# Optimization experiments

Measured on AMD Instinct MI355X. Metric: run time of the kernel, lower is better.

## Reference

```python
import jax, jax.numpy as jnp
import numpy as np

B, S, H, E, TOPK = 4, 4096, 2048, 128, 8


def setup_inputs() -> dict:
    key = jax.random.key(0)
    k1, k2 = jax.random.split(key)
    hidden_states = jax.random.normal(k1, (B, S, H), dtype=jnp.float32)
    weight = jax.random.normal(k2, (E, H), dtype=jnp.float32) * 0.02
    return {"hidden_states": hidden_states, "weight": weight, "top_k": TOPK}


def reference(hidden_states, weight, top_k):
    x = hidden_states.reshape(-1, weight.shape[1])              # [T, H]
    router_logits = jnp.einsum('th,eh->te', x, weight)          # [T, E]
    router_probs = jax.nn.softmax(router_logits.astype(jnp.float32), axis=-1)
    router_top_value, router_indices = jax.lax.top_k(router_probs, top_k)  # [T, K]
    router_top_value = router_top_value / jnp.sum(router_top_value, axis=-1, keepdims=True)
    router_top_value = router_top_value.astype(router_logits.dtype)
    return (router_logits, router_top_value, router_indices)
```

## Files before the change

### kernel.cpp

```cpp
#include <hip/hip_runtime.h>
#include <hip/hip_bf16.h>
#include <hip/hip_fp16.h>

#define NTOK 16384
#define HDIM 2048
#define NEXP 128
#define KSEL 8
#define NCAND 16
#define DELTA_GAP 1e-4f
#define LO_SCALE 2048.0f
#define LO_INV (1.0f/2048.0f)

typedef _Float16 half8  __attribute__((ext_vector_type(8)));
typedef float    f32x4  __attribute__((ext_vector_type(4)));

__global__ __launch_bounds__(256) void w_convert(
    const float* __restrict__ w, _Float16* __restrict__ whp, _Float16* __restrict__ wlp)
{
    const int e = blockIdx.x;
    const int k = threadIdx.x * 8;
    const float* src = w + (size_t)e * HDIM + k;
    const f32x4 v0 = *reinterpret_cast<const f32x4*>(src);
    const f32x4 v1 = *reinterpret_cast<const f32x4*>(src + 4);
    float vv[8] = {v0[0], v0[1], v0[2], v0[3], v1[0], v1[1], v1[2], v1[3]};
    half8 h, lo;
#pragma unroll
    for (int j = 0; j < 8; ++j) {
        const _Float16 hj = (_Float16)vv[j];
        h[j]  = hj;
        lo[j] = (_Float16)((vv[j] - (float)hj) * LO_SCALE);
    }
    const int ks = k >> 5;
    const int eg = e >> 4;
    const int l  = (e & 15) | (((k >> 3) & 3) << 4);
    const size_t di = ((size_t)(ks * 8 + eg) * 64 + l) * 8;
    *reinterpret_cast<half8*>(whp + di) = h;
    *reinterpret_cast<half8*>(wlp + di) = lo;
}

__global__ __launch_bounds__(256, 2) void gemm3_nolds(
    const float* __restrict__ x,
    const _Float16* __restrict__ whp, const _Float16* __restrict__ wlp,
    float* __restrict__ logits, float* __restrict__ topv, float* __restrict__ topi,
    int* __restrict__ cand, int* __restrict__ flag)
{
    __shared__ f32x4 red[4][2][8][64];

    const int tid = threadIdx.x;
    const int l   = tid & 63;
    const int q   = tid >> 6;
    const int t0  = blockIdx.x * 32;

    const float* xrow0 = x + (size_t)(t0 + (l & 15)) * HDIM + q * 512 + 8 * (l >> 4);
    const float* xrow1 = xrow0 + (size_t)16 * HDIM;
    const _Float16* wqh = whp + (size_t)q * 16 * 8 * 512;
    const _Float16* wql = wlp + (size_t)q * 16 * 8 * 512;

    f32x4 acc[2][8], acc2[2][8];
#pragma unroll
    for (int ms = 0; ms < 2; ++ms)
#pragma unroll
        for (int eg = 0; eg < 8; ++eg) {
            acc[ms][eg]  = (f32x4){0.f, 0.f, 0.f, 0.f};
            acc2[ms][eg] = (f32x4){0.f, 0.f, 0.f, 0.f};
        }

    f32x4 acur[2][2];
    acur[0][0] = *reinterpret_cast<const f32x4*>(xrow0);
    acur[0][1] = *reinterpret_cast<const f32x4*>(xrow0 + 4);
    acur[1][0] = *reinterpret_cast<const f32x4*>(xrow1);
    acur[1][1] = *reinterpret_cast<const f32x4*>(xrow1 + 4);

#pragma unroll 1
    for (int s = 0; s < 16; ++s) {
        half8 bh[8], bl[8];
#pragma unroll
        for (int eg = 0; eg < 8; ++eg) {
            bh[eg] = *reinterpret_cast<const half8*>(wqh + ((size_t)s * 8 + eg) * 512 + l * 8);
            bl[eg] = *reinterpret_cast<const half8*>(wql + ((size_t)s * 8 + eg) * 512 + l * 8);
        }

        f32x4 anxt[2][2];
        if (s + 1 < 16) {
            anxt[0][0] = *reinterpret_cast<const f32x4*>(xrow0 + (s + 1) * 32);
            anxt[0][1] = *reinterpret_cast<const f32x4*>(xrow0 + (s + 1) * 32 + 4);
            anxt[1][0] = *reinterpret_cast<const f32x4*>(xrow1 + (s + 1) * 32);
            anxt[1][1] = *reinterpret_cast<const f32x4*>(xrow1 + (s + 1) * 32 + 4);
        }

        half8 ah[2], al[2];
#pragma unroll
        for (int ms = 0; ms < 2; ++ms)
#pragma unroll
            for (int j = 0; j < 4; ++j) {
                const _Float16 h0 = (_Float16)acur[ms][0][j];
                const _Float16 h1 = (_Float16)acur[ms][1][j];
                ah[ms][j]     = h0;
                ah[ms][4 + j] = h1;
                al[ms][j]     = (_Float16)((acur[ms][0][j] - (float)h0) * LO_SCALE);
                al[ms][4 + j] = (_Float16)((acur[ms][1][j] - (float)h1) * LO_SCALE);
            }

#pragma unroll
        for (int eg = 0; eg < 8; ++eg)
#pragma unroll
            for (int ms = 0; ms < 2; ++ms) {
                acc[ms][eg]  = __builtin_amdgcn_mfma_f32_16x16x32_f16(ah[ms], bh[eg], acc[ms][eg],  0, 0, 0);
                acc2[ms][eg] = __builtin_amdgcn_mfma_f32_16x16x32_f16(ah[ms], bl[eg], acc2[ms][eg], 0, 0, 0);
                acc2[ms][eg] = __builtin_amdgcn_mfma_f32_16x16x32_f16(al[ms], bh[eg], acc2[ms][eg], 0, 0, 0);
            }

        if (s + 1 < 16) {
#pragma unroll
            for (int ms = 0; ms < 2; ++ms)
#pragma unroll
                for (int h = 0; h < 2; ++h)
                    acur[ms][h] = anxt[ms][h];
        }
    }

#pragma unroll
    for (int ms = 0; ms < 2; ++ms)
#pragma unroll
        for (int eg = 0; eg < 8; ++eg)
            red[q][ms][eg][l] = acc[ms][eg] + acc2[ms][eg] * LO_INV;
    __syncthreads();

    const int ms_w = q >> 1;
    f32x4 v[8];
#pragma unroll
    for (int eg = 0; eg < 8; ++eg) {
        f32x4 s0 = red[0][ms_w][eg][l];
        s0 += red[1][ms_w][eg][l];
        s0 += red[2][ms_w][eg][l];
        s0 += red[3][ms_w][eg][l];
        v[eg] = s0;
    }

    const int grp  = l >> 4;
    const int ln16 = l & 15;
    const int r0   = 2 * (q & 1);
    const float NEG = -__builtin_inff();

#pragma unroll
    for (int rr = 0; rr < 4; ++rr) {
        if (rr != r0 && rr != r0 + 1) continue;
        const int t = t0 + ms_w * 16 + 4 * grp + rr;
        float vr[8];
#pragma unroll
        for (int f = 0; f < 8; ++f) {
            vr[f] = v[f][rr];
            logits[(size_t)t * NEXP + 16 * f + ln16] = vr[f];
        }

        unsigned selm = 0u;
        int   mycand = 0;
        float mycv   = 0.0f;
#pragma unroll
        for (int k = 0; k < NCAND; ++k) {
            float lv = NEG; int le = 0;
#pragma unroll
            for (int f = 0; f < 8; ++f) {
                const float c = ((selm >> f) & 1u) ? NEG : vr[f];
                if (c > lv) { lv = c; le = 16 * f + ln16; }
            }
            float cv = lv; int ce = le;
#pragma unroll
            for (int off = 8; off > 0; off >>= 1) {
                const float ov = __shfl_xor(cv, off, 16);
                const int   oe = __shfl_xor(ce, off, 16);
                if (ov > cv || (ov == cv && oe < ce)) { cv = ov; ce = oe; }
            }
            if (ln16 == k) { mycand = ce; mycv = cv; }
            if ((ce & 15) == ln16) selm |= 1u << (ce >> 4);
        }

        const float nv = __shfl(mycv, ln16 + 1, 16);
        int fl = (ln16 <= 8 && (mycv - nv) < DELTA_GAP) ? 1 : 0;
#pragma unroll
        for (int off = 8; off > 0; off >>= 1)
            fl |= __shfl_xor(fl, off, 16);

        const float m = __shfl(mycv, 0, 16);
        const float p = (ln16 < KSEL) ? expf(mycv - m) : 0.0f;
        float ps = p;
#pragma unroll
        for (int off = 8; off > 0; off >>= 1)
            ps += __shfl_xor(ps, off, 16);

        cand[(size_t)t * NCAND + ln16] = mycand;
        if (ln16 < KSEL) {
            topv[(size_t)t * KSEL + ln16] = p / ps;
            topi[(size_t)t * KSEL + ln16] = (float)mycand;
        }
        if (ln16 == 0) flag[t] = fl;
    }
}

__global__ __launch_bounds__(256) void refine_flagged(
    const float* __restrict__ x, const float* __restrict__ w,
    const int* __restrict__ cand, const int* __restrict__ flag,
    float* __restrict__ topv, float* __restrict__ topi)
{
    const int l = threadIdx.x & 63;
    const int t = (int)((blockIdx.x * 256u + threadIdx.x) >> 6);
    if (!flag[t]) return;

    const int myid = cand[(size_t)t * NCAND + (l & 15)];
    const float* xrow = x + (size_t)t * HDIM;

    double xd[32];
#pragma unroll
    for (int i = 0; i < 8; ++i) {
        const f32x4 xv = *reinterpret_cast<const f32x4*>(xrow + i * 256 + l * 4);
#pragma unroll
        for (int j = 0; j < 4; ++j) xd[i * 4 + j] = (double)xv[j];
    }

    double part[NCAND];
    int    cid[NCAND];
#pragma unroll
    for (int c = 0; c < NCAND; ++c) {
        const int eid = __shfl(myid, c);
        cid[c] = eid;
        const float* wrow = w + (size_t)eid * HDIM;
        double s0 = 0.0, s1 = 0.0, s2 = 0.0, s3 = 0.0;
#pragma unroll
        for (int i = 0; i < 8; ++i) {
            const f32x4 wv4 = *reinterpret_cast<const f32x4*>(wrow + i * 256 + l * 4);
            s0 = fma(xd[i * 4 + 0], (double)wv4[0], s0);
            s1 = fma(xd[i * 4 + 1], (double)wv4[1], s1);
            s2 = fma(xd[i * 4 + 2], (double)wv4[2], s2);
            s3 = fma(xd[i * 4 + 3], (double)wv4[3], s3);
        }
        part[c] = (s0 + s1) + (s2 + s3);
    }

#pragma unroll
    for (int off = 32; off > 0; off >>= 1)
#pragma unroll
        for (int c = 0; c < NCAND; ++c)
            part[c] += __shfl_xor(part[c], off);

    unsigned selm = 0u;
    double m = 0.0, kv = 0.0;
    int ki = 0;
    float psum = 0.0f;
#pragma unroll
    for (int k = 0; k < KSEL; ++k) {
        double bv = -__builtin_inf(); int bi = 0x7fffffff; int bc = 0;
#pragma unroll
        for (int c = 0; c < NCAND; ++c) {
            if (!((selm >> c) & 1u)) {
                if (part[c] > bv || (part[c] == bv && cid[c] < bi)) {
                    bv = part[c]; bi = cid[c]; bc = c;
                }
            }
        }
        if (k == 0) m = bv;
        psum += expf((float)(bv - m));
        if (l == k) { kv = bv; ki = bi; }
        selm |= 1u << bc;
    }

    if (l < KSEL) {
        topv[(size_t)t * KSEL + l] = expf((float)(kv - m)) / psum;
        topi[(size_t)t * KSEL + l] = (float)ki;
    }
}

#define BM 64
#define BK 32
#define BSTRIDE (BK + 4)
__global__ __launch_bounds__(256) void router_fused(
    const float* __restrict__ x, const float* __restrict__ w,
    float* __restrict__ logits, float* __restrict__ topv, float* __restrict__ topi)
{
    __shared__ float Bs[NEXP][BSTRIDE];
    const int tid = threadIdx.x;
    const int tn = tid & 15, tm = tid >> 4;
    const int row0 = blockIdx.x * BM;
    const int kc = tid & 7, cr = tid >> 3;

    double acc[4][8];
#pragma unroll
    for (int i = 0; i < 4; ++i)
#pragma unroll
        for (int j = 0; j < 8; ++j) acc[i][j] = 0.0;

    const float* xp[4];
#pragma unroll
    for (int i = 0; i < 4; ++i) xp[i] = x + (size_t)(row0 + tm + 16 * i) * HDIM;

    float4 rb[4];
#pragma unroll
    for (int p = 0; p < 4; ++p)
        rb[p] = *reinterpret_cast<const float4*>(&w[(size_t)(cr + 32 * p) * HDIM + kc * 4]);

    for (int k0 = 0; k0 < HDIM; k0 += BK) {
        __syncthreads();
#pragma unroll
        for (int p = 0; p < 4; ++p)
            *reinterpret_cast<float4*>(&Bs[cr + 32 * p][kc * 4]) = rb[p];
        __syncthreads();
        if (k0 + BK < HDIM) {
#pragma unroll
            for (int p = 0; p < 4; ++p)
                rb[p] = *reinterpret_cast<const float4*>(
                    &w[(size_t)(cr + 32 * p) * HDIM + (k0 + BK) + kc * 4]);
        }
#pragma unroll 4
        for (int k4 = 0; k4 < BK; k4 += 4) {
            float4 a4[4], b4[8];
#pragma unroll
            for (int i = 0; i < 4; ++i)
                a4[i] = *reinterpret_cast<const float4*>(&xp[i][k0 + k4]);
#pragma unroll
            for (int j = 0; j < 8; ++j)
                b4[j] = *reinterpret_cast<const float4*>(&Bs[tn + 16 * j][k4]);
#pragma unroll
            for (int kk = 0; kk < 4; ++kk) {
                double bd[8];
#pragma unroll
                for (int j = 0; j < 8; ++j) bd[j] = (double)((const float*)&b4[j])[kk];
#pragma unroll
                for (int i = 0; i < 4; ++i) {
                    const double ad = (double)((const float*)&a4[i])[kk];
#pragma unroll
                    for (int j = 0; j < 8; ++j) acc[i][j] = fma(ad, bd[j], acc[i][j]);
                }
            }
        }
    }
#pragma unroll
    for (int i = 0; i < 4; ++i) {
        float* orow = logits + (size_t)(row0 + tm + 16 * i) * NEXP;
#pragma unroll
        for (int j = 0; j < 8; ++j) orow[tn + 16 * j] = (float)acc[i][j];
    }
    for (int i = 0; i < 4; ++i) {
        const int t = row0 + tm + 16 * i;
        unsigned sel = 0u;
        double m = 0.0, kv = 0.0;
        int ki = 0;
        const double NEGD = -__builtin_inf();
#pragma unroll
        for (int k = 0; k < KSEL; ++k) {
            double lv = NEGD; int le = 0;
#pragma unroll
            for (int j = 0; j < 8; ++j) {
                const double v = (sel >> j) & 1u ? NEGD : acc[i][j];
                if (v > lv) { lv = v; le = tn + 16 * j; }
            }
            double cv = lv; int ce = le;
#pragma unroll
            for (int off = 8; off > 0; off >>= 1) {
                const double ov = __shfl_xor(cv, off, 16);
                const int    oe = __shfl_xor(ce, off, 16);
                if (ov > cv || (ov == cv && oe < ce)) { cv = ov; ce = oe; }
            }
            if (k == 0) m = cv;
            if (tn == k) { kv = cv; ki = ce; }
            if ((ce & 15) == tn) sel |= 1u << (ce >> 4);
        }
        float z = 0.0f;
#pragma unroll
        for (int j = 0; j < 8; ++j) z += expf((float)(acc[i][j] - m));
#pragma unroll
        for (int off = 8; off > 0; off >>= 1) z += __shfl_xor(z, off, 16);
        const float p = (tn < KSEL) ? expf((float)(kv - m)) / z : 0.0f;
        float ps = p;
#pragma unroll
        for (int off = 8; off > 0; off >>= 1) ps += __shfl_xor(ps, off, 16);
        if (tn < KSEL) {
            topv[(size_t)t * KSEL + tn] = p / ps;
            topi[(size_t)t * KSEL + tn] = (float)ki;
        }
    }
}

extern "C" void kernel_launch(void* const* d_in, const int* in_sizes, int n_in,
                              void* d_out, int out_size, void* d_ws, size_t ws_size,
                              hipStream_t stream) {
    const float* x = (const float*)d_in[0];
    const float* w = (const float*)d_in[1];

    float* out    = (float*)d_out;
    float* logits = out;
    float* topv   = out + (size_t)NTOK * NEXP;
    float* topi   = topv + (size_t)NTOK * KSEL;

    const size_t plane = (size_t)NEXP * HDIM;
    const size_t need  = plane * 2 * sizeof(_Float16)
                       + (size_t)NTOK * NCAND * sizeof(int)
                       + (size_t)NTOK * sizeof(int);
    if (ws_size >= need) {
        _Float16* whp = (_Float16*)d_ws;
        _Float16* wlp = whp + plane;
        int* cand = (int*)(wlp + plane);
        int* flag = cand + (size_t)NTOK * NCAND;
        w_convert<<<NEXP, 256, 0, stream>>>(w, whp, wlp);
        gemm3_nolds<<<NTOK / 32, 256, 0, stream>>>(x, whp, wlp, logits, topv, topi, cand, flag);
        refine_flagged<<<NTOK / 4, 256, 0, stream>>>(x, w, cand, flag, topv, topi);
    } else {
        router_fused<<<NTOK / BM, 256, 0, stream>>>(x, w, logits, topv, topi);
    }
}
```

Measured before the change: 81.57 us.

## Split GEMM waves over expert halves and K halves to cut registers

Each wave previously covered all 128 experts over a quarter of K. It now covers 64 experts over half of K, which halves the accumulator registers and allows the launch bound to rise from 2 to 3 blocks per SM. The shared-memory reduction shrinks from a four-way sum to a two-way sum. The software prefetch of the next x slice is removed, and refine_flagged now keeps x as float and converts to double at each use, which further lowers register pressure. The risk is that each wave reads twice as many x values per MFMA and loses the load/compute overlap the prefetch provided.

```diff
diff --git a/kernel.cpp b/kernel.cpp
--- a/kernel.cpp
+++ b/kernel.cpp
@@ -38,109 +38,94 @@
     *reinterpret_cast<half8*>(wlp + di) = lo;
 }
 
-__global__ __launch_bounds__(256, 2) void gemm3_nolds(
+__global__ __launch_bounds__(256, 3) void gemm3_split(
     const float* __restrict__ x,
     const _Float16* __restrict__ whp, const _Float16* __restrict__ wlp,
     float* __restrict__ logits, float* __restrict__ topv, float* __restrict__ topi,
     int* __restrict__ cand, int* __restrict__ flag)
 {
-    __shared__ f32x4 red[4][2][8][64];
+    __shared__ f32x4 red[2][2][2][4][64];
 
     const int tid = threadIdx.x;
     const int l   = tid & 63;
-    const int q   = tid >> 6;
+    const int W   = tid >> 6;
+    const int eh  = W & 1;
+    const int kh  = W >> 1;
     const int t0  = blockIdx.x * 32;
 
-    const float* xrow0 = x + (size_t)(t0 + (l & 15)) * HDIM + q * 512 + 8 * (l >> 4);
+    const float* xrow0 = x + (size_t)(t0 + (l & 15)) * HDIM + kh * 1024 + 8 * (l >> 4);
     const float* xrow1 = xrow0 + (size_t)16 * HDIM;
-    const _Float16* wqh = whp + (size_t)q * 16 * 8 * 512;
-    const _Float16* wql = wlp + (size_t)q * 16 * 8 * 512;
-
-    f32x4 acc[2][8], acc2[2][8];
+
+    f32x4 acc[2][4], acc2[2][4];
 #pragma unroll
     for (int ms = 0; ms < 2; ++ms)
 #pragma unroll
-        for (int eg = 0; eg < 8; ++eg) {
-            acc[ms][eg]  = (f32x4){0.f, 0.f, 0.f, 0.f};
-            acc2[ms][eg] = (f32x4){0.f, 0.f, 0.f, 0.f};
-        }
-
-    f32x4 acur[2][2];
-    acur[0][0] = *reinterpret_cast<const f32x4*>(xrow0);
-    acur[0][1] = *reinterpret_cast<const f32x4*>(xrow0 + 4);
-    acur[1][0] = *reinterpret_cast<const f32x4*>(xrow1);
-    acur[1][1] = *reinterpret_cast<const f32x4*>(xrow1 + 4);
+        for (int g = 0; g < 4; ++g) {
+            acc[ms][g]  = (f32x4){0.f, 0.f, 0.f, 0.f};
+            acc2[ms][g] = (f32x4){0.f, 0.f, 0.f, 0.f};
+        }
 
 #pragma unroll 1
-    for (int s = 0; s < 16; ++s) {
-        half8 bh[8], bl[8];
-#pragma unroll
-        for (int eg = 0; eg < 8; ++eg) {
-            bh[eg] = *reinterpret_cast<const half8*>(wqh + ((size_t)s * 8 + eg) * 512 + l * 8);
-            bl[eg] = *reinterpret_cast<const half8*>(wql + ((size_t)s * 8 + eg) * 512 + l * 8);
-        }
-
-        f32x4 anxt[2][2];
-        if (s + 1 < 16) {
-            anxt[0][0] = *reinterpret_cast<const f32x4*>(xrow0 + (s + 1) * 32);
-            anxt[0][1] = *reinterpret_cast<const f32x4*>(xrow0 + (s + 1) * 32 + 4);
-            anxt[1][0] = *reinterpret_cast<const f32x4*>(xrow1 + (s + 1) * 32);
-            anxt[1][1] = *reinterpret_cast<const f32x4*>(xrow1 + (s + 1) * 32 + 4);
-        }
+    for (int s = 0; s < 32; ++s) {
+        const int ks = kh * 32 + s;
+
+        half8 bh[4], bl[4];
+#pragma unroll
+        for (int g = 0; g < 4; ++g) {
+            const size_t off = (size_t)(ks * 8 + 4 * eh + g) * 512 + l * 8;
+            bh[g] = *reinterpret_cast<const half8*>(whp + off);
+            bl[g] = *reinterpret_cast<const half8*>(wlp + off);
+        }
+
+        const f32x4 a00 = *reinterpret_cast<const f32x4*>(xrow0 + s * 32);
+        const f32x4 a01 = *reinterpret_cast<const f32x4*>(xrow0 + s * 32 + 4);
+        const f32x4 a10 = *reinterpret_cast<const f32x4*>(xrow1 + s * 32);
+        const f32x4 a11 = *reinterpret_cast<const f32x4*>(xrow1 + s * 32 + 4);
 
         half8 ah[2], al[2];
 #pragma unroll
-        for (int ms = 0; ms < 2; ++ms)
-#pragma unroll
-            for (int j = 0; j < 4; ++j) {
-                const _Float16 h0 = (_Float16)acur[ms][0][j];
-                const _Float16 h1 = (_Float16)acur[ms][1][j];
-                ah[ms][j]     = h0;
-                ah[ms][4 + j] = h1;
-                al[ms][j]     = (_Float16)((acur[ms][0][j] - (float)h0) * LO_SCALE);
-                al[ms][4 + j] = (_Float16)((acur[ms][1][j] - (float)h1) * LO_SCALE);
-            }
-
-#pragma unroll
-        for (int eg = 0; eg < 8; ++eg)
+        for (int j = 0; j < 4; ++j) {
+            const _Float16 h00 = (_Float16)a00[j];
+            const _Float16 h01 = (_Float16)a01[j];
+            const _Float16 h10 = (_Float16)a10[j];
+            const _Float16 h11 = (_Float16)a11[j];
+            ah[0][j]     = h00;
+            ah[0][4 + j] = h01;
+            ah[1][j]     = h10;
+            ah[1][4 + j] = h11;
+            al[0][j]     = (_Float16)((a00[j] - (float)h00) * LO_SCALE);
+            al[0][4 + j] = (_Float16)((a01[j] - (float)h01) * LO_SCALE);
+            al[1][j]     = (_Float16)((a10[j] - (float)h10) * LO_SCALE);
+            al[1][4 + j] = (_Float16)((a11[j] - (float)h11) * LO_SCALE);
+        }
+
+#pragma unroll
+        for (int g = 0; g < 4; ++g)
 #pragma unroll
             for (int ms = 0; ms < 2; ++ms) {
-                acc[ms][eg]  = __builtin_amdgcn_mfma_f32_16x16x32_f16(ah[ms], bh[eg], acc[ms][eg],  0, 0, 0);
-                acc2[ms][eg] = __builtin_amdgcn_mfma_f32_16x16x32_f16(ah[ms], bl[eg], acc2[ms][eg], 0, 0, 0);
-                acc2[ms][eg] = __builtin_amdgcn_mfma_f32_16x16x32_f16(al[ms], bh[eg], acc2[ms][eg], 0, 0, 0);
-            }
-
-        if (s + 1 < 16) {
-#pragma unroll
-            for (int ms = 0; ms < 2; ++ms)
-#pragma unroll
-                for (int h = 0; h < 2; ++h)
-                    acur[ms][h] = anxt[ms][h];
-        }
+                acc[ms][g]  = __builtin_amdgcn_mfma_f32_16x16x32_f16(ah[ms], bh[g], acc[ms][g],  0, 0, 0);
+                acc2[ms][g] = __builtin_amdgcn_mfma_f32_16x16x32_f16(ah[ms], bl[g], acc2[ms][g], 0, 0, 0);
+                acc2[ms][g] = __builtin_amdgcn_mfma_f32_16x16x32_f16(al[ms], bh[g], acc2[ms][g], 0, 0, 0);
+            }
     }
 
 #pragma unroll
     for (int ms = 0; ms < 2; ++ms)
 #pragma unroll
-        for (int eg = 0; eg < 8; ++eg)
-            red[q][ms][eg][l] = acc[ms][eg] + acc2[ms][eg] * LO_INV;
+        for (int g = 0; g < 4; ++g)
+            red[kh][eh][ms][g][l] = acc[ms][g] + acc2[ms][g] * LO_INV;
     __syncthreads();
 
-    const int ms_w = q >> 1;
-    f32x4 v[8];
-#pragma unroll
-    for (int eg = 0; eg < 8; ++eg) {
-        f32x4 s0 = red[0][ms_w][eg][l];
-        s0 += red[1][ms_w][eg][l];
-        s0 += red[2][ms_w][eg][l];
-        s0 += red[3][ms_w][eg][l];
-        v[eg] = s0;
-    }
-
+    const int ms_w = W >> 1;
+    const int r0   = 2 * (W & 1);
     const int grp  = l >> 4;
     const int ln16 = l & 15;
-    const int r0   = 2 * (q & 1);
     const float NEG = -__builtin_inff();
+
+    f32x4 v[8];
+#pragma unroll
+    for (int f = 0; f < 8; ++f)
+        v[f] = red[0][f >> 2][ms_w][f & 3][l] + red[1][f >> 2][ms_w][f & 3][l];
 
 #pragma unroll
     for (int rr = 0; rr < 4; ++rr) {
@@ -209,13 +194,10 @@
     const int myid = cand[(size_t)t * NCAND + (l & 15)];
     const float* xrow = x + (size_t)t * HDIM;
 
-    double xd[32];
-#pragma unroll
-    for (int i = 0; i < 8; ++i) {
-        const f32x4 xv = *reinterpret_cast<const f32x4*>(xrow + i * 256 + l * 4);
-#pragma unroll
-        for (int j = 0; j < 4; ++j) xd[i * 4 + j] = (double)xv[j];
-    }
+    f32x4 xv[8];
+#pragma unroll
+    for (int i = 0; i < 8; ++i)
+        xv[i] = *reinterpret_cast<const f32x4*>(xrow + i * 256 + l * 4);
 
     double part[NCAND];
     int    cid[NCAND];
@@ -228,10 +210,10 @@
 #pragma unroll
         for (int i = 0; i < 8; ++i) {
             const f32x4 wv4 = *reinterpret_cast<const f32x4*>(wrow + i * 256 + l * 4);
-            s0 = fma(xd[i * 4 + 0], (double)wv4[0], s0);
-            s1 = fma(xd[i * 4 + 1], (double)wv4[1], s1);
-            s2 = fma(xd[i * 4 + 2], (double)wv4[2], s2);
-            s3 = fma(xd[i * 4 + 3], (double)wv4[3], s3);
+            s0 = fma((double)xv[i][0], (double)wv4[0], s0);
+            s1 = fma((double)xv[i][1], (double)wv4[1], s1);
+            s2 = fma((double)xv[i][2], (double)wv4[2], s2);
+            s3 = fma((double)xv[i][3], (double)wv4[3], s3);
         }
         part[c] = (s0 + s1) + (s2 + s3);
     }
@@ -400,7 +382,7 @@
         int* cand = (int*)(wlp + plane);
         int* flag = cand + (size_t)NTOK * NCAND;
         w_convert<<<NEXP, 256, 0, stream>>>(w, whp, wlp);
-        gemm3_nolds<<<NTOK / 32, 256, 0, stream>>>(x, whp, wlp, logits, topv, topi, cand, flag);
+        gemm3_split<<<NTOK / 32, 256, 0, stream>>>(x, whp, wlp, logits, topv, topi, cand, flag);
         refine_flagged<<<NTOK / 4, 256, 0, stream>>>(x, w, cand, flag, topv, topi);
     } else {
         router_fused<<<NTOK / BM, 256, 0, stream>>>(x, w, logits, topv, topi);
```

New measurement: 115.8 us. +42.0%, slower.
